# Performance work log

Measured on AMD Instinct MI355X. Metric: run time of the kernel, lower is better.

## Reference

```python
import jax, jax.numpy as jnp
import numpy as np

BATCH, TIMESTEPS, DIM, OUT = 64, 512, 1024, 1024


def setup_inputs() -> dict:
    key = jax.random.key(0)
    k1, k2, k3, k4, k5, k6 = jax.random.split(key, 6)
    # glorot-normal-ish scales for params
    def glorot(k, shape):
        fan_in, fan_out = shape[0], shape[-1]
        std = (2.0 / (fan_in + fan_out)) ** 0.5
        return jax.random.normal(k, shape, dtype=jnp.float32) * std
    return {
        "inputs": jax.random.normal(k1, (BATCH, TIMESTEPS, DIM), dtype=jnp.float32),
        "prev_state": jax.random.normal(k2, (BATCH, OUT), dtype=jnp.float32),
        "Wa": glorot(k3, (OUT, OUT)),
        "Ua": glorot(k4, (DIM, OUT)),
        "Va": glorot(k5, (OUT, 1)),
        "Ba": glorot(k6, (1, OUT)),
    }


def reference(inputs, prev_state, Wa, Ua, Va, Ba):
    # WaS: [B, 1, OUT] broadcast over timesteps
    WaS = jnp.einsum("bo,op->bp", prev_state, Wa)[:, None, :]
    # UaH: [B, T, OUT]
    UaH = jnp.einsum("btd,do->bto", inputs, Ua)
    scores = jnp.tanh(UaH + WaS + Ba)            # [B, T, OUT]
    scores = jax.nn.relu(scores @ Va)            # [B, T, 1]
    sm = jax.nn.softmax(scores, axis=1)          # softmax over timesteps
    context_vector = jnp.sum(inputs * sm, axis=1)  # [B, DIM]
    return context_vector
```

## Files before the change

kernel.cpp:

```cpp
#include <hip/hip_runtime.h>


typedef _Float16 h8 __attribute__((ext_vector_type(8)));
typedef float f16v __attribute__((ext_vector_type(16)));

__device__ __forceinline__ float tanh_fast(float x) {
    float e = __expf(2.0f * x);
    return 1.0f - 2.0f * __builtin_amdgcn_rcpf(e + 1.0f);
}

__global__ __launch_bounds__(256) void k_pack_ua(const float* __restrict__ Ua,
                                                 _Float16* __restrict__ B16) {
    int t = blockIdx.x * 256 + threadIdx.x;
    int nn = t & 31, kg = (t >> 5) & 1, ks = (t >> 6) & 63, nt = t >> 12;
    int n = (nt << 5) + nn;
    int kbase = (ks << 4) + (kg << 3);
    h8 v;
#pragma unroll
    for (int j = 0; j < 8; ++j) v[j] = (_Float16)Ua[(size_t)(kbase + j) * 1024 + n];
    *(h8*)(B16 + ((size_t)t << 3)) = v;
}

__global__ __launch_bounds__(256) void k_pack_a(const float* __restrict__ inputs,
                                                _Float16* __restrict__ A16) {
    const int bx = blockIdx.x, t = threadIdx.x;
    const int rl = t >> 3, oc0 = t & 7;
    const float4* src = (const float4*)(inputs + (((size_t)bx * 32 + rl) << 10));
    h8* dst = (h8*)A16 + ((size_t)bx << 12) + rl;
#pragma unroll
    for (int i = 0; i < 16; ++i) {
        int o = oc0 + (i << 3);
        float4 v0 = src[o * 2], v1 = src[o * 2 + 1];
        h8 ov = { (_Float16)v0.x, (_Float16)v0.y, (_Float16)v0.z, (_Float16)v0.w,
                  (_Float16)v1.x, (_Float16)v1.y, (_Float16)v1.z, (_Float16)v1.w };
        dst[((o >> 1) << 6) + ((o & 1) << 5)] = ov;
    }
}

__global__ __launch_bounds__(256) void k_was_part(const float* __restrict__ ps,
                                                  const float* __restrict__ Wa,
                                                  float* __restrict__ part) {
    int ic = blockIdx.x >> 2, psl = blockIdx.x & 3;
    int tid = threadIdx.x, wv = tid >> 6, lane = tid & 63;
    int p4 = psl * 64 + lane;
    const float4* Wa4 = (const float4*)Wa;
    float4* part4 = (float4*)part;
#pragma unroll 1
    for (int c = 0; c < 4; ++c) {
        int o0 = ic * 128 + c * 32;
        float4 w[32];
#pragma unroll
        for (int o = 0; o < 32; ++o) w[o] = Wa4[(size_t)(o0 + o) * 256 + p4];
#pragma unroll 1
        for (int bb = 0; bb < 16; ++bb) {
            int b = wv * 16 + bb;
            const float* psb = ps + b * 1024 + o0;
            size_t oidx = (size_t)((ic << 6) + b) * 256 + p4;
            float4 a;
            if (c == 0) { a.x = a.y = a.z = a.w = 0.f; }
            else        { a = part4[oidx]; }
#pragma unroll
            for (int o = 0; o < 32; ++o) {
                float s = psb[o];
                a.x += s * w[o].x; a.y += s * w[o].y;
                a.z += s * w[o].z; a.w += s * w[o].w;
            }
            part4[oidx] = a;
        }
    }
}

__global__ __launch_bounds__(256) void k_was_reduce(const float* __restrict__ part,
                                                    const float* __restrict__ Ba,
                                                    float* __restrict__ wsWaS) {
    int b = blockIdx.x, tid = threadIdx.x;
    const float4* p4 = (const float4*)part;
    float4 acc = ((const float4*)Ba)[tid];
#pragma unroll
    for (int ic = 0; ic < 8; ++ic) {
        float4 v = p4[((ic << 6) + b) * 256 + tid];
        acc.x += v.x; acc.y += v.y; acc.z += v.z; acc.w += v.w;
    }
    ((float4*)wsWaS)[b * 256 + tid] = acc;
}

__global__ __launch_bounds__(256, 2) void k_fused_gemm(
    const _Float16* __restrict__ A16, const _Float16* __restrict__ B16,
    const float* __restrict__ wsWaS, const float* __restrict__ Va,
    float* __restrict__ scores)
{
    __shared__ float scoreSh[64];
    const int tid = threadIdx.x;
    const int lane = tid & 63, wv = tid >> 6;
    const int l31 = lane & 31, lhi = lane >> 5;
    const int r0 = blockIdx.x * 64;
    const int rb0 = blockIdx.x * 2;
    const int b = r0 >> 9;

    if (tid < 64) scoreSh[tid] = 0.0f;
    __syncthreads();

    const h8* A8 = (const h8*)A16;
    const h8* B8 = (const h8*)B16;
    const h8* aBase = A8 + ((size_t)rb0 << 12) + lane;

    for (int pass = 0; pass < 2; ++pass) {
        const int ntb = (pass << 4) + (wv << 2);
        const h8* bBase = B8 + ((size_t)ntb << 12) + lane;

        f16v acc[2][4];
#pragma unroll
        for (int rt = 0; rt < 2; ++rt)
#pragma unroll
            for (int ct = 0; ct < 4; ++ct)
#pragma unroll
                for (int e = 0; e < 16; ++e) acc[rt][ct][e] = 0.0f;

        h8 af[4][2], bf[2][4];
#pragma unroll
        for (int p = 0; p < 4; ++p)
#pragma unroll
            for (int rt = 0; rt < 2; ++rt) af[p][rt] = aBase[rt * 4096 + p * 64];
#pragma unroll
        for (int ct = 0; ct < 4; ++ct) bf[0][ct] = bBase[ct * 4096];

#pragma unroll 4
        for (int ks = 0; ks < 64; ++ks) {
            const int cur = ks & 1, nxt = cur ^ 1, ra = ks & 3;
            h8 a0 = af[ra][0], a1 = af[ra][1];
            if (ks < 60) {
                const int o = (ks + 4) << 6;
                af[ra][0] = aBase[o];
                af[ra][1] = aBase[4096 + o];
            }
            if (ks < 63) {
                const int o = (ks + 1) << 6;
#pragma unroll
                for (int ct = 0; ct < 4; ++ct) bf[nxt][ct] = bBase[ct * 4096 + o];
            }
#pragma unroll
            for (int ct = 0; ct < 4; ++ct) {
                acc[0][ct] = __builtin_amdgcn_mfma_f32_32x32x16_f16(a0, bf[cur][ct], acc[0][ct], 0, 0, 0);
                acc[1][ct] = __builtin_amdgcn_mfma_f32_32x32x16_f16(a1, bf[cur][ct], acc[1][ct], 0, 0, 0);
            }
        }

        float wsv[4], vav[4];
#pragma unroll
        for (int ct = 0; ct < 4; ++ct) {
            int n = (ntb + ct) << 5 | l31;
            wsv[ct] = wsWaS[b * 1024 + n];
            vav[ct] = Va[n];
        }
#pragma unroll
        for (int rt = 0; rt < 2; ++rt) {
#pragma unroll
            for (int i = 0; i < 16; ++i) {
                float s = 0.0f;
#pragma unroll
                for (int ct = 0; ct < 4; ++ct)
                    s += tanh_fast(acc[rt][ct][i] + wsv[ct]) * vav[ct];
                s += __shfl_xor(s, 1);
                s += __shfl_xor(s, 2);
                s += __shfl_xor(s, 4);
                s += __shfl_xor(s, 8);
                s += __shfl_xor(s, 16);
                if (l31 == 0) {
                    int row = rt * 32 + (i & 3) + ((i >> 2) << 3) + (lhi << 2);
                    atomicAdd(&scoreSh[row], s);
                }
            }
        }
    }
    __syncthreads();
    if (tid < 64) scores[r0 + tid] = fmaxf(scoreSh[tid], 0.0f);
}

__global__ __launch_bounds__(256) void k_softmax(const float* __restrict__ scores,
                                                 float* __restrict__ sm) {
    int b = blockIdx.x, tid = threadIdx.x;
    __shared__ float red[256];
    const float* sb = scores + b * 512;
    float s0 = sb[tid], s1 = sb[tid + 256];
    red[tid] = fmaxf(s0, s1);
    __syncthreads();
    for (int st = 128; st > 0; st >>= 1) {
        if (tid < st) red[tid] = fmaxf(red[tid], red[tid + st]);
        __syncthreads();
    }
    float m = red[0];
    __syncthreads();
    float e0 = __expf(s0 - m), e1 = __expf(s1 - m);
    red[tid] = e0 + e1;
    __syncthreads();
    for (int st = 128; st > 0; st >>= 1) {
        if (tid < st) red[tid] += red[tid + st];
        __syncthreads();
    }
    float inv = 1.0f / red[0];
    sm[b * 512 + tid] = e0 * inv;
    sm[b * 512 + 256 + tid] = e1 * inv;
}

__global__ __launch_bounds__(256) void k_ctx(const _Float16* __restrict__ A16,
                                             const float* __restrict__ sm,
                                             float* __restrict__ out) {
    const int bx = blockIdx.x, b = blockIdx.y;
    const int tid = threadIdx.x, wv = tid >> 6, lane = tid & 63;
    const int l31 = lane & 31, lhi = lane >> 5;
    const h8* A8 = (const h8*)A16;
    const int ksl = bx * 4 + wv;
    float facc[8];
#pragma unroll
    for (int j = 0; j < 8; ++j) facc[j] = 0.0f;
    const float* smb = sm + b * 512;
#pragma unroll 4
    for (int rbl = 0; rbl < 16; ++rbl) {
        h8 x = A8[(((size_t)(b * 16 + rbl) << 6) + ksl) * 64 + lane];
        float wgt = smb[rbl * 32 + l31];
#pragma unroll
        for (int j = 0; j < 8; ++j) facc[j] += wgt * (float)x[j];
    }
#pragma unroll
    for (int m = 1; m < 32; m <<= 1)
#pragma unroll
        for (int j = 0; j < 8; ++j) facc[j] += __shfl_xor(facc[j], m);
    if (l31 == 0) {
        int oct = bx * 8 + wv * 2 + lhi;
        float* o = out + b * 1024 + oct * 8;
#pragma unroll
        for (int j = 0; j < 8; ++j) o[j] = facc[j];
    }
}

extern "C" void kernel_launch(void* const* d_in, const int* in_sizes, int n_in,
                              void* d_out, int out_size, void* d_ws, size_t ws_size,
                              hipStream_t stream) {
    const float* inputs = (const float*)d_in[0];
    const float* prev   = (const float*)d_in[1];
    const float* Wa     = (const float*)d_in[2];
    const float* Ua     = (const float*)d_in[3];
    const float* Va     = (const float*)d_in[4];
    const float* Ba     = (const float*)d_in[5];
    float* out = (float*)d_out;

    char* ws = (char*)d_ws;
    _Float16* A16   = (_Float16*)(ws);
    _Float16* B16   = (_Float16*)(ws + (64u << 20));
    float* wasPart  = (float*)(ws + (66u << 20));
    float* wsWaS    = (float*)(ws + (68u << 20));
    float* scores   = (float*)(ws + (68u << 20) + (256u << 10));
    float* sm       = (float*)(ws + (68u << 20) + (384u << 10));

    hipLaunchKernelGGL(k_pack_ua,    dim3(512),    dim3(256), 0, stream, Ua, B16);
    hipLaunchKernelGGL(k_pack_a,     dim3(1024),   dim3(256), 0, stream, inputs, A16);
    hipLaunchKernelGGL(k_was_part,   dim3(32),     dim3(256), 0, stream, prev, Wa, wasPart);
    hipLaunchKernelGGL(k_was_reduce, dim3(64),     dim3(256), 0, stream, wasPart, Ba, wsWaS);
    hipLaunchKernelGGL(k_fused_gemm, dim3(512),    dim3(256), 0, stream, A16, B16, wsWaS, Va, scores);
    hipLaunchKernelGGL(k_softmax,    dim3(64),     dim3(256), 0, stream, scores, sm);
    hipLaunchKernelGGL(k_ctx,        dim3(16, 64), dim3(256), 0, stream, A16, sm, out);
}
```

Baseline: 367.3 us.

## Stage A tiles in LDS with 512-thread blocks covering 128 rows

```diff
diff --git a/kernel.cpp b/kernel.cpp
--- a/kernel.cpp
+++ b/kernel.cpp
@@ -24,16 +24,18 @@
 __global__ __launch_bounds__(256) void k_pack_a(const float* __restrict__ inputs,
                                                 _Float16* __restrict__ A16) {
     const int bx = blockIdx.x, t = threadIdx.x;
-    const int rl = t >> 3, oc0 = t & 7;
-    const float4* src = (const float4*)(inputs + (((size_t)bx * 32 + rl) << 10));
-    h8* dst = (h8*)A16 + ((size_t)bx << 12) + rl;
+    h8* dst = (h8*)A16 + ((size_t)bx << 12);
+    const float* src = inputs + ((size_t)bx << 15);
 #pragma unroll
     for (int i = 0; i < 16; ++i) {
-        int o = oc0 + (i << 3);
-        float4 v0 = src[o * 2], v1 = src[o * 2 + 1];
-        h8 ov = { (_Float16)v0.x, (_Float16)v0.y, (_Float16)v0.z, (_Float16)v0.w,
-                  (_Float16)v1.x, (_Float16)v1.y, (_Float16)v1.z, (_Float16)v1.w };
-        dst[((o >> 1) << 6) + ((o & 1) << 5)] = ov;
+        int p = (i << 8) + t;
+        int ks = p >> 6, l = p & 63;
+        int row = l & 31;
+        int k = (ks << 4) + ((l >> 5) << 3);
+        const float4* s = (const float4*)(src + ((size_t)row << 10) + k);
+        float4 v0 = s[0], v1 = s[1];
+        dst[p] = (h8){ (_Float16)v0.x, (_Float16)v0.y, (_Float16)v0.z, (_Float16)v0.w,
+                       (_Float16)v1.x, (_Float16)v1.y, (_Float16)v1.z, (_Float16)v1.w };
     }
 }
 
@@ -84,96 +86,117 @@
     ((float4*)wsWaS)[b * 256 + tid] = acc;
 }
 
-__global__ __launch_bounds__(256, 2) void k_fused_gemm(
+__global__ __launch_bounds__(512, 2) void k_fused_gemm(
     const _Float16* __restrict__ A16, const _Float16* __restrict__ B16,
     const float* __restrict__ wsWaS, const float* __restrict__ Va,
     float* __restrict__ scores)
 {
-    __shared__ float scoreSh[64];
+    __shared__ uint4 Albuf[2][2048];
+    __shared__ float scoreSh[128];
     const int tid = threadIdx.x;
     const int lane = tid & 63, wv = tid >> 6;
     const int l31 = lane & 31, lhi = lane >> 5;
-    const int r0 = blockIdx.x * 64;
-    const int rb0 = blockIdx.x * 2;
+    const int r0 = blockIdx.x * 128;
     const int b = r0 >> 9;
-
-    if (tid < 64) scoreSh[tid] = 0.0f;
-    __syncthreads();
-
-    const h8* A8 = (const h8*)A16;
+    const uint4* Ag = (const uint4*)A16 + ((size_t)blockIdx.x << 14);
     const h8* B8 = (const h8*)B16;
-    const h8* aBase = A8 + ((size_t)rb0 << 12) + lane;
+
+    if (tid < 128) scoreSh[tid] = 0.0f;
 
     for (int pass = 0; pass < 2; ++pass) {
-        const int ntb = (pass << 4) + (wv << 2);
+        const int ntb = (pass << 4) + (wv << 1);
         const h8* bBase = B8 + ((size_t)ntb << 12) + lane;
 
-        f16v acc[2][4];
-#pragma unroll
-        for (int rt = 0; rt < 2; ++rt)
-#pragma unroll
-            for (int ct = 0; ct < 4; ++ct)
+        f16v acc[4][2];
+#pragma unroll
+        for (int rt = 0; rt < 4; ++rt)
+#pragma unroll
+            for (int ct = 0; ct < 2; ++ct)
 #pragma unroll
                 for (int e = 0; e < 16; ++e) acc[rt][ct][e] = 0.0f;
 
-        h8 af[4][2], bf[2][4];
-#pragma unroll
-        for (int p = 0; p < 4; ++p)
-#pragma unroll
-            for (int rt = 0; rt < 2; ++rt) af[p][rt] = aBase[rt * 4096 + p * 64];
-#pragma unroll
-        for (int ct = 0; ct < 4; ++ct) bf[0][ct] = bBase[ct * 4096];
-
-#pragma unroll 4
-        for (int ks = 0; ks < 64; ++ks) {
-            const int cur = ks & 1, nxt = cur ^ 1, ra = ks & 3;
-            h8 a0 = af[ra][0], a1 = af[ra][1];
-            if (ks < 60) {
-                const int o = (ks + 4) << 6;
-                af[ra][0] = aBase[o];
-                af[ra][1] = aBase[4096 + o];
-            }
-            if (ks < 63) {
-                const int o = (ks + 1) << 6;
-#pragma unroll
-                for (int ct = 0; ct < 4; ++ct) bf[nxt][ct] = bBase[ct * 4096 + o];
-            }
-#pragma unroll
-            for (int ct = 0; ct < 4; ++ct) {
-                acc[0][ct] = __builtin_amdgcn_mfma_f32_32x32x16_f16(a0, bf[cur][ct], acc[0][ct], 0, 0, 0);
-                acc[1][ct] = __builtin_amdgcn_mfma_f32_32x32x16_f16(a1, bf[cur][ct], acc[1][ct], 0, 0, 0);
-            }
-        }
-
-        float wsv[4], vav[4];
-#pragma unroll
-        for (int ct = 0; ct < 4; ++ct) {
-            int n = (ntb + ct) << 5 | l31;
+        uint4 vA[4];
+#pragma unroll
+        for (int i = 0; i < 4; ++i) {
+            int p = tid + (i << 9);
+            int f = p >> 6, l = p & 63;
+            vA[i] = Ag[(((f >> 3) << 12)) + ((f & 7) << 6) + l];
+        }
+#pragma unroll
+        for (int i = 0; i < 4; ++i) Albuf[0][tid + (i << 9)] = vA[i];
+        __syncthreads();
+
+        h8 bf[2][2];
+#pragma unroll
+        for (int ct = 0; ct < 2; ++ct) bf[0][ct] = bBase[ct << 12];
+
+#pragma unroll 1
+        for (int kc = 0; kc < 8; ++kc) {
+            const int buf = kc & 1;
+            if (kc < 7) {
+                const int kb = (kc + 1) << 3;
+#pragma unroll
+                for (int i = 0; i < 4; ++i) {
+                    int p = tid + (i << 9);
+                    int f = p >> 6, l = p & 63;
+                    vA[i] = Ag[(((f >> 3) << 12)) + ((kb + (f & 7)) << 6) + l];
+                }
+            }
+#pragma unroll
+            for (int ks8 = 0; ks8 < 8; ++ks8) {
+                const int ks = (kc << 3) + ks8;
+                const int cur = ks & 1, nxt = cur ^ 1;
+                h8 af[4];
+#pragma unroll
+                for (int rt = 0; rt < 4; ++rt)
+                    af[rt] = *(const h8*)&Albuf[buf][((rt << 3) + ks8) * 64 + lane];
+                if (ks < 63) {
+                    const int o = (ks + 1) << 6;
+#pragma unroll
+                    for (int ct = 0; ct < 2; ++ct)
+                        bf[nxt][ct] = bBase[(ct << 12) + o];
+                }
+#pragma unroll
+                for (int rt = 0; rt < 4; ++rt)
+#pragma unroll
+                    for (int ct = 0; ct < 2; ++ct)
+                        acc[rt][ct] = __builtin_amdgcn_mfma_f32_32x32x16_f16(
+                            af[rt], bf[cur][ct], acc[rt][ct], 0, 0, 0);
+            }
+            if (kc < 7) {
+#pragma unroll
+                for (int i = 0; i < 4; ++i) Albuf[buf ^ 1][tid + (i << 9)] = vA[i];
+            }
+            __syncthreads();
+        }
+
+        float wsv[2], vav[2];
+#pragma unroll
+        for (int ct = 0; ct < 2; ++ct) {
+            int n = ((ntb + ct) << 5) | l31;
             wsv[ct] = wsWaS[b * 1024 + n];
             vav[ct] = Va[n];
         }
 #pragma unroll
-        for (int rt = 0; rt < 2; ++rt) {
+        for (int rt = 0; rt < 4; ++rt) {
 #pragma unroll
             for (int i = 0; i < 16; ++i) {
-                float s = 0.0f;
-#pragma unroll
-                for (int ct = 0; ct < 4; ++ct)
-                    s += tanh_fast(acc[rt][ct][i] + wsv[ct]) * vav[ct];
+                float s = tanh_fast(acc[rt][0][i] + wsv[0]) * vav[0]
+                        + tanh_fast(acc[rt][1][i] + wsv[1]) * vav[1];
                 s += __shfl_xor(s, 1);
                 s += __shfl_xor(s, 2);
                 s += __shfl_xor(s, 4);
                 s += __shfl_xor(s, 8);
                 s += __shfl_xor(s, 16);
                 if (l31 == 0) {
-                    int row = rt * 32 + (i & 3) + ((i >> 2) << 3) + (lhi << 2);
+                    int row = (rt << 5) + (i & 3) + ((i >> 2) << 3) + (lhi << 2);
                     atomicAdd(&scoreSh[row], s);
                 }
             }
         }
     }
     __syncthreads();
-    if (tid < 64) scores[r0 + tid] = fmaxf(scoreSh[tid], 0.0f);
+    if (tid < 128) scores[r0 + tid] = fmaxf(scoreSh[tid], 0.0f);
 }
 
 __global__ __launch_bounds__(256) void k_softmax(const float* __restrict__ scores,
@@ -256,7 +279,7 @@
     hipLaunchKernelGGL(k_pack_a,     dim3(1024),   dim3(256), 0, stream, inputs, A16);
     hipLaunchKernelGGL(k_was_part,   dim3(32),     dim3(256), 0, stream, prev, Wa, wasPart);
     hipLaunchKernelGGL(k_was_reduce, dim3(64),     dim3(256), 0, stream, wasPart, Ba, wsWaS);
-    hipLaunchKernelGGL(k_fused_gemm, dim3(512),    dim3(256), 0, stream, A16, B16, wsWaS, Va, scores);
+    hipLaunchKernelGGL(k_fused_gemm, dim3(256),    dim3(512), 0, stream, A16, B16, wsWaS, Va, scores);
     hipLaunchKernelGGL(k_softmax,    dim3(64),     dim3(256), 0, stream, scores, sm);
     hipLaunchKernelGGL(k_ctx,        dim3(16, 64), dim3(256), 0, stream, A16, sm, out);
 }
```

After: 392.0 us. 6.7% more time.
